# Kernel optimization log

Measured on AMD Instinct MI355X. Metric: run time of the kernel, lower is better.

The kernel has to match this reference:

```python
import jax, jax.numpy as jnp
import numpy as np

B, C, T, H, W, E, K = 2, 256, 16, 32, 32, 4, 2


def setup_inputs() -> dict:
    key = jax.random.key(0)
    ks = jax.random.split(key, 5)
    x = jax.random.normal(ks[0], (B, C, T, H, W), dtype=jnp.float32)
    # gate: Conv3d(dim, E, 1) -> weight [E, C], bias [E]
    gate_w = jax.random.normal(ks[1], (E, C), dtype=jnp.float32) * 0.02
    gate_b = jnp.zeros((E,), dtype=jnp.float32)
    # experts_layer1: Conv3d(dim, dim*E, 1) -> weight [E*C, C], bias [E*C]
    w1 = jax.random.normal(ks[2], (E * C, C), dtype=jnp.float32) * 0.02
    b1 = jnp.zeros((E * C,), dtype=jnp.float32)
    # experts_layer2: Conv3d(dim*E, dim*E, 1, groups=E) -> per-expert [C, C]
    w2 = jax.random.normal(ks[3], (E, C, C), dtype=jnp.float32) * 0.02
    b2 = jnp.zeros((E, C), dtype=jnp.float32)
    return {"x": x, "gate_w": gate_w, "gate_b": gate_b,
            "w1": w1, "b1": b1, "w2": w2, "b2": b2}


def reference(x, gate_w, gate_b, w1, b1, w2, b2):
    # gating: 1x1x1 conv == channel contraction; logits [B,T,H,W,E]
    logits = jnp.einsum('bcthw,ec->bthwe', x, gate_w) + gate_b
    vals, idx = jax.lax.top_k(logits, K)              # [B,T,H,W,K]
    wk = jax.nn.softmax(vals, axis=-1).astype(x.dtype)
    # scatter top-k softmax weights back into E slots (zeros elsewhere)
    weights = jnp.sum(jax.nn.one_hot(idx, E, dtype=x.dtype) * wk[..., None],
                      axis=-2)                        # [B,T,H,W,E]
    # layer1 (dense 1x1x1 conv) + SiLU; output channels = E*C
    h = jax.nn.silu(jnp.einsum('bcthw,oc->bothw', x, w1)
                    + b1[None, :, None, None, None])
    h = h.reshape(B, E, C, T, H, W)
    # layer2: grouped 1x1x1 conv, one [C,C] matmul per expert
    expert_out = (jnp.einsum('becthw,eoc->beothw', h, w2)
                  + b2[None, :, :, None, None, None])  # [B,E,C,T,H,W]
    # weighted combine over experts + residual
    out = jnp.einsum('becthw,bthwe->bcthw', expert_out, weights)
    return out + x
```

## Files before the change

kernel.cpp:

```cpp
#include <hip/hip_runtime.h>
#include <hip/hip_bf16.h>


#define C_DIM 256
#define S_DIM 16384
#define E_DIM 4
#define MT 64
#define XST 264
#define OST 68
#define WFRAG_ELEMS 262144

typedef __attribute__((ext_vector_type(8))) short bf16x8;
typedef __attribute__((ext_vector_type(4))) short short4v;
typedef __attribute__((ext_vector_type(4))) float f32x4;

__device__ __forceinline__ short bfq(float f) {
  __hip_bfloat16 h = __float2bfloat16(f);
  return *(short*)&h;
}

__global__ __launch_bounds__(256) void prepack_kernel(
    const float* __restrict__ w1, const float* __restrict__ w2,
    __hip_bfloat16* __restrict__ dst)
{
  int o = blockIdx.x * 256 + threadIdx.x;
  int half = o >> 18;
  int idx = o & (WFRAG_ELEMS - 1);
  int j    = idx & 7;
  int lane = (idx >> 3) & 63;
  int kc   = (idx >> 9) & 7;
  int nt   = (idx >> 12) & 15;
  int e    = (idx >> 16) & 3;
  const float* src = half ? w2 : w1;
  int si = (e*256 + nt*16 + (lane & 15))*256 + kc*32 + (lane >> 4)*8 + j;
  dst[o] = __float2bfloat16(src[si]);
}

__global__ __launch_bounds__(512, 4) void moe_fused_kernel(
    const float* __restrict__ x,
    const float* __restrict__ gate_w,
    const float* __restrict__ gate_b,
    const float* __restrict__ b1,
    const float* __restrict__ b2,
    const __hip_bfloat16* __restrict__ wp,
    float* __restrict__ out)
{
  __shared__ __align__(16) char pool[256 * OST * 4];
  __shared__ float Wgt[MT * 4];
  __shared__ double GateP[512];

  short* XsS = (short*)pool;
  short* HsS = (short*)(pool + MT * XST * 2);
  float* Os  = (float*)pool;

  const int tid  = threadIdx.x;
  const int lane = tid & 63;
  const int wv   = tid >> 6;
  const int r    = lane & 15;
  const int q    = lane >> 4;

  const int g  = blockIdx.x;
  const int b  = g >> 8;
  const int s0 = (g & 255) * MT;
  const float* xb = x + (size_t)b * C_DIM * S_DIM + s0;

  {
    const int p4 = (tid & 15) * 4;
    const int cg = tid >> 4;
#pragma unroll
    for (int cc = 0; cc < 2; ++cc) {
      const int c0 = (cc*32 + cg) * 4;
      const float4 v0 = *(const float4*)(xb + (size_t)(c0+0)*S_DIM + p4);
      const float4 v1 = *(const float4*)(xb + (size_t)(c0+1)*S_DIM + p4);
      const float4 v2 = *(const float4*)(xb + (size_t)(c0+2)*S_DIM + p4);
      const float4 v3 = *(const float4*)(xb + (size_t)(c0+3)*S_DIM + p4);
      *(short4v*)(XsS + (p4+0)*XST + c0) = (short4v){bfq(v0.x), bfq(v1.x), bfq(v2.x), bfq(v3.x)};
      *(short4v*)(XsS + (p4+1)*XST + c0) = (short4v){bfq(v0.y), bfq(v1.y), bfq(v2.y), bfq(v3.y)};
      *(short4v*)(XsS + (p4+2)*XST + c0) = (short4v){bfq(v0.z), bfq(v1.z), bfq(v2.z), bfq(v3.z)};
      *(short4v*)(XsS + (p4+3)*XST + c0) = (short4v){bfq(v0.w), bfq(v1.w), bfq(v2.w), bfq(v3.w)};
    }
  }

  {
    const int p  = lane;
    const int e  = wv & 3;
    const int ch = wv >> 2;
    const float* gw = gate_w + e * C_DIM + ch * 128;
    const float* xr = xb + p + (size_t)(ch * 128) * S_DIM;
    double a0 = 0.0, a1 = 0.0, a2 = 0.0, a3 = 0.0;
#pragma unroll 4
    for (int c = 0; c < 128; c += 4) {
      a0 += (double)xr[(size_t)(c+0) * S_DIM] * (double)gw[c+0];
      a1 += (double)xr[(size_t)(c+1) * S_DIM] * (double)gw[c+1];
      a2 += (double)xr[(size_t)(c+2) * S_DIM] * (double)gw[c+2];
      a3 += (double)xr[(size_t)(c+3) * S_DIM] * (double)gw[c+3];
    }
    GateP[(ch*64 + p)*4 + e] = (a0 + a1) + (a2 + a3);
  }
  __syncthreads();

  if (tid < MT) {
    const int p = tid;
    float l[4];
#pragma unroll
    for (int e = 0; e < 4; ++e)
      l[e] = (float)(GateP[p*4 + e] + GateP[(64 + p)*4 + e] + (double)gate_b[e]);
    int i1 = 0; float v1 = l[0];
    if (l[1] > v1) { v1 = l[1]; i1 = 1; }
    if (l[2] > v1) { v1 = l[2]; i1 = 2; }
    if (l[3] > v1) { v1 = l[3]; i1 = 3; }
    float v2 = -3.0e38f; int i2 = 0;
    if (i1 != 0 && l[0] > v2) { v2 = l[0]; i2 = 0; }
    if (i1 != 1 && l[1] > v2) { v2 = l[1]; i2 = 1; }
    if (i1 != 2 && l[2] > v2) { v2 = l[2]; i2 = 2; }
    if (i1 != 3 && l[3] > v2) { v2 = l[3]; i2 = 3; }
    const float wA = 1.0f / (1.0f + __expf(v2 - v1));
    const float wB = 1.0f - wA;
    Wgt[p*4+0] = (i1 == 0) ? wA : ((i2 == 0) ? wB : 0.0f);
    Wgt[p*4+1] = (i1 == 1) ? wA : ((i2 == 1) ? wB : 0.0f);
    Wgt[p*4+2] = (i1 == 2) ? wA : ((i2 == 2) ? wB : 0.0f);
    Wgt[p*4+3] = (i1 == 3) ? wA : ((i2 == 3) ? wB : 0.0f);
  }
  __syncthreads();

  const short* W1P = (const short*)wp;
  const short* W2P = (const short*)wp + WFRAG_ELEMS;

  f32x4 oacc[4][2];
#pragma unroll
  for (int i = 0; i < 4; ++i)
#pragma unroll
    for (int j = 0; j < 2; ++j) oacc[i][j] = (f32x4){0.f, 0.f, 0.f, 0.f};

  for (int e = 0; e < E_DIM; ++e) {
    f32x4 hacc[4][2];
#pragma unroll
    for (int i = 0; i < 4; ++i)
#pragma unroll
      for (int j = 0; j < 2; ++j) hacc[i][j] = (f32x4){0.f, 0.f, 0.f, 0.f};

    {
      const short* w1e = W1P + ((e*16 + wv*2)*8)*512 + lane*8;
      bf16x8 bw[2][2];
#pragma unroll
      for (int t = 0; t < 2; ++t) bw[0][t] = *(const bf16x8*)(w1e + (t*8 + 0)*512);
#pragma unroll
      for (int kc = 0; kc < 8; ++kc) {
        if (kc < 7) {
#pragma unroll
          for (int t = 0; t < 2; ++t)
            bw[(kc+1)&1][t] = *(const bf16x8*)(w1e + (t*8 + kc + 1)*512);
        }
        bf16x8 a[4];
#pragma unroll
        for (int Mt = 0; Mt < 4; ++Mt)
          a[Mt] = *(const bf16x8*)(XsS + (Mt*16 + r)*XST + kc*32 + q*8);
#pragma unroll
        for (int Mt = 0; Mt < 4; ++Mt)
#pragma unroll
          for (int t = 0; t < 2; ++t)
            hacc[Mt][t] = __builtin_amdgcn_mfma_f32_16x16x32_bf16(a[Mt], bw[kc&1][t], hacc[Mt][t], 0, 0, 0);
      }
    }

    const short* w2e = W2P + ((e*16 + wv*2)*8)*512 + lane*8;
    bf16x8 cw[2][2];
#pragma unroll
    for (int t = 0; t < 2; ++t) cw[0][t] = *(const bf16x8*)(w2e + (t*8 + 0)*512);

    {
      float wreg[4][4];
#pragma unroll
      for (int Mt = 0; Mt < 4; ++Mt)
#pragma unroll
        for (int reg = 0; reg < 4; ++reg)
          wreg[Mt][reg] = Wgt[(Mt*16 + q*4 + reg)*4 + e];
#pragma unroll
      for (int t = 0; t < 2; ++t) {
        const int n = wv*32 + t*16 + r;
        const float bias = b1[e*256 + n];
#pragma unroll
        for (int Mt = 0; Mt < 4; ++Mt)
#pragma unroll
          for (int reg = 0; reg < 4; ++reg) {
            const float z = hacc[Mt][t][reg] + bias;
            const float s = __builtin_amdgcn_rcpf(1.0f + __expf(-z));
            const float h = z * s * wreg[Mt][reg];
            HsS[(Mt*16 + q*4 + reg)*XST + n] = bfq(h);
          }
      }
    }
    __syncthreads();

    {
#pragma unroll
      for (int kc = 0; kc < 8; ++kc) {
        if (kc < 7) {
#pragma unroll
          for (int t = 0; t < 2; ++t)
            cw[(kc+1)&1][t] = *(const bf16x8*)(w2e + (t*8 + kc + 1)*512);
        }
        bf16x8 a[4];
#pragma unroll
        for (int Mt = 0; Mt < 4; ++Mt)
          a[Mt] = *(const bf16x8*)(HsS + (Mt*16 + r)*XST + kc*32 + q*8);
#pragma unroll
        for (int Mt = 0; Mt < 4; ++Mt)
#pragma unroll
          for (int t = 0; t < 2; ++t)
            oacc[Mt][t] = __builtin_amdgcn_mfma_f32_16x16x32_bf16(a[Mt], cw[kc&1][t], oacc[Mt][t], 0, 0, 0);
      }
    }
    __syncthreads();
  }

  {
    float b2v[2][4];
#pragma unroll
    for (int t = 0; t < 2; ++t) {
      const int c = wv*32 + t*16 + r;
#pragma unroll
      for (int e = 0; e < 4; ++e) b2v[t][e] = b2[e*256 + c];
    }
#pragma unroll
    for (int Mt = 0; Mt < 4; ++Mt) {
      f32x4 wv4[4];
#pragma unroll
      for (int reg = 0; reg < 4; ++reg)
        wv4[reg] = *(const f32x4*)(&Wgt[(Mt*16 + q*4 + reg)*4]);
#pragma unroll
      for (int t = 0; t < 2; ++t) {
        f32x4 v = oacc[Mt][t];
#pragma unroll
        for (int reg = 0; reg < 4; ++reg)
          v[reg] += wv4[reg][0]*b2v[t][0] + wv4[reg][1]*b2v[t][1]
                  + wv4[reg][2]*b2v[t][2] + wv4[reg][3]*b2v[t][3];
        *(f32x4*)(Os + (size_t)(wv*32 + t*16 + r)*OST + Mt*16 + q*4) = v;
      }
    }
  }
  __syncthreads();

  {
    const int p4 = (tid & 15) * 4;
    const int cg = tid >> 4;
    float* ob = out + (size_t)b * C_DIM * S_DIM + s0;
#pragma unroll
    for (int cc = 0; cc < 8; ++cc) {
      const int c = cc*32 + cg;
      const f32x4  o  = *(const f32x4*)(Os + (size_t)c*OST + p4);
      const float4 xr = *(const float4*)(xb + (size_t)c*S_DIM + p4);
      float4 res;
      res.x = o[0] + xr.x; res.y = o[1] + xr.y;
      res.z = o[2] + xr.z; res.w = o[3] + xr.w;
      *(float4*)(ob + (size_t)c*S_DIM + p4) = res;
    }
  }
}

extern "C" void kernel_launch(void* const* d_in, const int* in_sizes, int n_in,
                              void* d_out, int out_size, void* d_ws, size_t ws_size,
                              hipStream_t stream)
{
  (void)in_sizes; (void)n_in; (void)out_size; (void)ws_size;
  const float* x      = (const float*)d_in[0];
  const float* gate_w = (const float*)d_in[1];
  const float* gate_b = (const float*)d_in[2];
  const float* w1     = (const float*)d_in[3];
  const float* b1     = (const float*)d_in[4];
  const float* w2     = (const float*)d_in[5];
  const float* b2     = (const float*)d_in[6];
  float* out = (float*)d_out;
  __hip_bfloat16* wpack = (__hip_bfloat16*)d_ws;

  prepack_kernel<<<2048, 256, 0, stream>>>(w1, w2, wpack);
  moe_fused_kernel<<<512, 512, 0, stream>>>(x, gate_w, gate_b, b1, b2, wpack, out);
}
```

Before: 136.9 us.

## Skip layer-1 GEMM rows for tokens not routed to each expert

```diff
diff --git a/kernel.cpp b/kernel.cpp
--- a/kernel.cpp
+++ b/kernel.cpp
@@ -36,6 +36,64 @@
   dst[o] = __float2bfloat16(src[si]);
 }
 
+template<int MTC>
+__device__ __forceinline__ void gemm1_sparse(
+    const short* XsS, short* HsS, const short* w1e, const float* b1e,
+    const unsigned char* plist_e, const float* wgtg_e,
+    int wv, int r, int q)
+{
+  f32x4 hacc[MTC][2];
+#pragma unroll
+  for (int i = 0; i < MTC; ++i)
+#pragma unroll
+    for (int j = 0; j < 2; ++j) hacc[i][j] = (f32x4){0.f, 0.f, 0.f, 0.f};
+
+  int aoff[MTC];
+#pragma unroll
+  for (int Mt = 0; Mt < MTC; ++Mt)
+    aoff[Mt] = (int)plist_e[Mt*16 + r] * XST;
+
+  bf16x8 bw[2][2];
+#pragma unroll
+  for (int t = 0; t < 2; ++t) bw[0][t] = *(const bf16x8*)(w1e + (t*8 + 0)*512);
+#pragma unroll
+  for (int kc = 0; kc < 8; ++kc) {
+    if (kc < 7) {
+#pragma unroll
+      for (int t = 0; t < 2; ++t)
+        bw[(kc+1)&1][t] = *(const bf16x8*)(w1e + (t*8 + kc + 1)*512);
+    }
+    bf16x8 a[MTC];
+#pragma unroll
+    for (int Mt = 0; Mt < MTC; ++Mt)
+      a[Mt] = *(const bf16x8*)(XsS + aoff[Mt] + kc*32 + q*8);
+#pragma unroll
+    for (int Mt = 0; Mt < MTC; ++Mt)
+#pragma unroll
+      for (int t = 0; t < 2; ++t)
+        hacc[Mt][t] = __builtin_amdgcn_mfma_f32_16x16x32_bf16(a[Mt], bw[kc&1][t], hacc[Mt][t], 0, 0, 0);
+  }
+
+#pragma unroll
+  for (int Mt = 0; Mt < MTC; ++Mt) {
+    const int g0 = Mt*16 + q*4;
+    const unsigned pw = *(const unsigned*)(plist_e + g0);
+    const f32x4 wg = *(const f32x4*)(wgtg_e + g0);
+#pragma unroll
+    for (int t = 0; t < 2; ++t) {
+      const int n = wv*32 + t*16 + r;
+      const float bias = b1e[n];
+#pragma unroll
+      for (int reg = 0; reg < 4; ++reg) {
+        const int p = (pw >> (8*reg)) & 255;
+        const float z = hacc[Mt][t][reg] + bias;
+        const float s = __builtin_amdgcn_rcpf(1.0f + __expf(-z));
+        HsS[p*XST + n] = bfq(z * s * wg[reg]);
+      }
+    }
+  }
+}
+
 __global__ __launch_bounds__(512, 4) void moe_fused_kernel(
     const float* __restrict__ x,
     const float* __restrict__ gate_w,
@@ -48,6 +106,10 @@
   __shared__ __align__(16) char pool[256 * OST * 4];
   __shared__ float Wgt[MT * 4];
   __shared__ double GateP[512];
+  __shared__ __align__(16) unsigned char plist[4][64];
+  __shared__ __align__(16) float WgtG[4][64];
+  __shared__ __align__(4)  unsigned char zlist[4][64];
+  __shared__ int mcnt[4];
 
   short* XsS = (short*)pool;
   short* HsS = (short*)(pool + MT * XST * 2);
@@ -123,6 +185,30 @@
   }
   __syncthreads();
 
+  if (wv < 4) {
+    const int e = wv;
+    const int p = lane;
+    const float w = Wgt[p*4 + e];
+    const bool sel = (w != 0.0f);
+    const unsigned long long mask = __ballot(sel);
+    const int below = __popcll(mask & ((1ull << p) - 1ull));
+    const int m = __popcll(mask);
+    const int pad = (((m + 15) >> 4) << 4) - m;
+    if (sel) {
+      plist[e][below] = (unsigned char)p;
+      WgtG[e][below]  = w;
+    } else {
+      const int zidx = p - below;
+      zlist[e][zidx] = (unsigned char)p;
+      if (zidx < pad) {
+        plist[e][m + zidx] = (unsigned char)p;
+        WgtG[e][m + zidx]  = 0.0f;
+      }
+    }
+    if (p == 0) mcnt[e] = m;
+  }
+  __syncthreads();
+
   const short* W1P = (const short*)wp;
   const short* W2P = (const short*)wp + WFRAG_ELEMS;
 
@@ -133,35 +219,15 @@
     for (int j = 0; j < 2; ++j) oacc[i][j] = (f32x4){0.f, 0.f, 0.f, 0.f};
 
   for (int e = 0; e < E_DIM; ++e) {
-    f32x4 hacc[4][2];
-#pragma unroll
-    for (int i = 0; i < 4; ++i)
-#pragma unroll
-      for (int j = 0; j < 2; ++j) hacc[i][j] = (f32x4){0.f, 0.f, 0.f, 0.f};
-
-    {
-      const short* w1e = W1P + ((e*16 + wv*2)*8)*512 + lane*8;
-      bf16x8 bw[2][2];
-#pragma unroll
-      for (int t = 0; t < 2; ++t) bw[0][t] = *(const bf16x8*)(w1e + (t*8 + 0)*512);
-#pragma unroll
-      for (int kc = 0; kc < 8; ++kc) {
-        if (kc < 7) {
-#pragma unroll
-          for (int t = 0; t < 2; ++t)
-            bw[(kc+1)&1][t] = *(const bf16x8*)(w1e + (t*8 + kc + 1)*512);
-        }
-        bf16x8 a[4];
-#pragma unroll
-        for (int Mt = 0; Mt < 4; ++Mt)
-          a[Mt] = *(const bf16x8*)(XsS + (Mt*16 + r)*XST + kc*32 + q*8);
-#pragma unroll
-        for (int Mt = 0; Mt < 4; ++Mt)
-#pragma unroll
-          for (int t = 0; t < 2; ++t)
-            hacc[Mt][t] = __builtin_amdgcn_mfma_f32_16x16x32_bf16(a[Mt], bw[kc&1][t], hacc[Mt][t], 0, 0, 0);
-      }
-    }
+    const int me = mcnt[e];
+    const int mt = __builtin_amdgcn_readfirstlane((me + 15) >> 4);
+    const short* w1e = W1P + ((e*16 + wv*2)*8)*512 + lane*8;
+    const float* b1e = b1 + e*256;
+
+    if      (mt == 2) gemm1_sparse<2>(XsS, HsS, w1e, b1e, plist[e], WgtG[e], wv, r, q);
+    else if (mt == 3) gemm1_sparse<3>(XsS, HsS, w1e, b1e, plist[e], WgtG[e], wv, r, q);
+    else if (mt == 4) gemm1_sparse<4>(XsS, HsS, w1e, b1e, plist[e], WgtG[e], wv, r, q);
+    else if (mt == 1) gemm1_sparse<1>(XsS, HsS, w1e, b1e, plist[e], WgtG[e], wv, r, q);
 
     const short* w2e = W2P + ((e*16 + wv*2)*8)*512 + lane*8;
     bf16x8 cw[2][2];
@@ -169,25 +235,11 @@
     for (int t = 0; t < 2; ++t) cw[0][t] = *(const bf16x8*)(w2e + (t*8 + 0)*512);
 
     {
-      float wreg[4][4];
-#pragma unroll
-      for (int Mt = 0; Mt < 4; ++Mt)
-#pragma unroll
-        for (int reg = 0; reg < 4; ++reg)
-          wreg[Mt][reg] = Wgt[(Mt*16 + q*4 + reg)*4 + e];
-#pragma unroll
-      for (int t = 0; t < 2; ++t) {
-        const int n = wv*32 + t*16 + r;
-        const float bias = b1[e*256 + n];
-#pragma unroll
-        for (int Mt = 0; Mt < 4; ++Mt)
-#pragma unroll
-          for (int reg = 0; reg < 4; ++reg) {
-            const float z = hacc[Mt][t][reg] + bias;
-            const float s = __builtin_amdgcn_rcpf(1.0f + __expf(-z));
-            const float h = z * s * wreg[Mt][reg];
-            HsS[(Mt*16 + q*4 + reg)*XST + n] = bfq(h);
-          }
+      const int zm = 64 - me;
+      const bf16x8 zz = {0,0,0,0,0,0,0,0};
+      for (int i = tid; i < zm*32; i += 512) {
+        const int row = zlist[e][i >> 5];
+        *(bf16x8*)(HsS + row*XST + (i & 31)*8) = zz;
       }
     }
     __syncthreads();
```

After: 136.6 us. Within noise of the previous version (-0.2%).
